# Kernel tuning notes

Measured on AMD Instinct MI355X. Metric: run time of the kernel, lower is better.

The kernel has to match this reference:

```python
import jax, jax.numpy as jnp
import numpy as np

SIZE_IN = 4096
SIZE_OUT = 4096
COEF = 8


def _make_mask(size_in, size_out, coef):
    # block-diagonal canceler: output row block i sees input column block i
    inp_sec = size_in // coef
    out_sec = size_out // coef
    row_block = np.arange(size_out) // out_sec  # [size_out]
    col_block = np.arange(size_in) // inp_sec   # [size_in]
    return (row_block[:, None] == col_block[None, :]).astype(np.float32)


def setup_inputs() -> dict:
    key = jax.random.key(0)
    kx, kw, kb = jax.random.split(key, 3)
    x = jax.random.normal(kx, (16384, SIZE_IN), dtype=jnp.float32)
    # kaiming_uniform_(a=sqrt(5)) on [size_out, size_in]: bound = sqrt(6/((1+5)*fan_in)) = 1/sqrt(fan_in)
    bound_w = 1.0 / np.sqrt(SIZE_IN)
    weights = jax.random.uniform(kw, (SIZE_OUT, SIZE_IN), minval=-bound_w, maxval=bound_w, dtype=jnp.float32)
    bound_b = 1.0 / np.sqrt(SIZE_IN)
    bias = jax.random.uniform(kb, (SIZE_OUT,), minval=-bound_b, maxval=bound_b, dtype=jnp.float32)
    mask = jnp.asarray(_make_mask(SIZE_IN, SIZE_OUT, COEF))
    return {"x": x, "weights": weights, "bias": bias, "mask": mask}


def reference(x, weights, bias, mask):
    # faithful to torch: full dense GEMM on the masked weight
    w = weights * mask                      # [size_out, size_in]
    return x @ w.T + bias                   # [batch, size_out]
```

## Files before the change

### kernel.cpp

```cpp
#include <hip/hip_runtime.h>
#include <hip/hip_bf16.h>


typedef __bf16 bf16x8 __attribute__((ext_vector_type(8)));
typedef float  f32x4  __attribute__((ext_vector_type(4)));

constexpr int LD = 4096;

__device__ __forceinline__ bf16x8 cvt8(f32x4 u, f32x4 v) {
    bf16x8 p;
    p[0] = (__bf16)u[0]; p[1] = (__bf16)u[1]; p[2] = (__bf16)u[2]; p[3] = (__bf16)u[3];
    p[4] = (__bf16)v[0]; p[5] = (__bf16)v[1]; p[6] = (__bf16)v[2]; p[7] = (__bf16)v[3];
    return p;
}

__device__ __forceinline__ void gload64(f32x4& a, f32x4& b, f32x4& c, f32x4& d,
                                        const void* p) {
    asm volatile("global_load_dwordx4 %0, %4, off\n\t"
                 "global_load_dwordx4 %1, %4, off offset:16\n\t"
                 "global_load_dwordx4 %2, %4, off offset:32\n\t"
                 "global_load_dwordx4 %3, %4, off offset:48"
                 : "=&v"(a), "=&v"(b), "=&v"(c), "=&v"(d) : "v"(p));
}
__device__ __forceinline__ void gload32(f32x4& a, f32x4& b, const void* p) {
    asm volatile("global_load_dwordx4 %0, %2, off\n\t"
                 "global_load_dwordx4 %1, %2, off offset:16"
                 : "=&v"(a), "=&v"(b) : "v"(p));
}

__global__ __launch_bounds__(256)
void pack_w(const float* __restrict__ w, __bf16* __restrict__ wt)
{
    const int g = blockIdx.x * 256 + threadIdx.x;
    const int base = g * 16;
    const int o = base >> 9;
    const int k = base & 511;
    const float* src = w + (size_t)o * LD + ((o >> 9) << 9) + k;
    f32x4 a = *(const f32x4*)(src);
    f32x4 b = *(const f32x4*)(src + 4);
    f32x4 c = *(const f32x4*)(src + 8);
    f32x4 d = *(const f32x4*)(src + 12);
    *(bf16x8*)(wt + base)     = cvt8(a, b);
    *(bf16x8*)(wt + base + 8) = cvt8(c, d);
}

#define VMW(N)                                                    \
    do {                                                          \
        asm volatile("s_waitcnt vmcnt(" #N ")" ::: "memory");     \
        __builtin_amdgcn_sched_barrier(0);                        \
    } while (0)

#define RD(TH, MH, KK)                                                        \
    do {                                                                      \
        const char* aB_ = smem + (TH) * 32768;                                \
        const char* bB_ = smem + 65536 + (TH) * 32768;                        \
        _Pragma("unroll")                                                     \
        for (int f = 0; f < 4; ++f) {                                         \
            const int row = wm * 128 + (MH) * 64 + f * 16 + arow;             \
            av[f] = *(const bf16x8*)(aB_ + row * 128 +                        \
                        (((KK) * 64 + ag * 16) ^ ((row & 7) << 4)));          \
        }                                                                     \
        _Pragma("unroll")                                                     \
        for (int n = 0; n < 4; ++n) {                                         \
            const int row = wn * 64 + n * 16 + arow;                          \
            bv[n] = *(const bf16x8*)(bB_ + row * 128 +                        \
                        (((KK) * 64 + ag * 16) ^ ((row & 7) << 4)));          \
        }                                                                     \
    } while (0)

#define FIRE(MH)                                                              \
    do {                                                                      \
        __builtin_amdgcn_s_barrier();                                         \
        asm volatile("s_waitcnt lgkmcnt(0)" ::: "memory");                    \
        __builtin_amdgcn_s_setprio(1);                                        \
        _Pragma("unroll")                                                     \
        for (int f = 0; f < 4; ++f)                                           \
            _Pragma("unroll")                                                 \
            for (int n = 0; n < 4; ++n)                                       \
                acc[(MH) * 4 + f][n] = __builtin_amdgcn_mfma_f32_16x16x32_bf16( \
                    av[f], bv[n], acc[(MH) * 4 + f][n], 0, 0, 0);             \
        __builtin_amdgcn_s_setprio(0);                                        \
        __builtin_amdgcn_s_barrier();                                         \
    } while (0)

__global__ __launch_bounds__(512, 2)
void fc_gemm(const float* __restrict__ x, const __bf16* __restrict__ wt,
             const float* __restrict__ bias, float* __restrict__ out)
{
    __shared__ __align__(16) char smem[131072];

    const int tid  = threadIdx.x;
    const int lane = tid & 63;
    const int wid  = tid >> 6;
    const int wm   = wid >> 2;
    const int wn   = wid & 3;

    const int bid  = blockIdx.x;
    const int j    = bid & 7;
    const int slot = bid >> 3;
    const int gm   = slot >> 1;
    const int gh   = slot & 1;
    const int koff    = j << 9;
    const int colbase = (j << 9) + (gh << 8);

    const int sRow = tid >> 2;
    const int sQ   = tid & 3;
    const int swzS = (sRow & 7) << 4;
    const int soA0 = sRow * 128 + ((sQ * 32)      ^ swzS);
    const int soA1 = sRow * 128 + ((sQ * 32 + 16) ^ swzS);
    const float*  xsB = x  + ((size_t)gm * 256 + sRow) * LD + koff + sQ * 16;
    const __bf16* wtB = wt + ((size_t)colbase + sRow) * 512 + sQ * 16;

    f32x4 stA[2][4];
    f32x4 stB[2][2];

    f32x4 acc[8][4];
#pragma unroll
    for (int i = 0; i < 8; ++i)
#pragma unroll
        for (int n = 0; n < 4; ++n)
            acc[i][n] = {0.f, 0.f, 0.f, 0.f};

    auto issueA = [&](int kt, int h) {
        gload64(stA[h][0], stA[h][1], stA[h][2], stA[h][3],
                xsB + (size_t)h * 128 * LD + kt * 64);
    };
    auto issueB = [&](int kt, int h) {
        gload32(stB[h][0], stB[h][1], wtB + (size_t)h * 65536 + kt * 64);
    };
    auto writeA = [&](int kt, int h) {
        char* base = smem + (kt & 1) * 32768 + h * 16384;
        *(bf16x8*)(base + soA0) = cvt8(stA[h][0], stA[h][1]);
        *(bf16x8*)(base + soA1) = cvt8(stA[h][2], stA[h][3]);
    };
    auto writeB = [&](int kt, int h) {
        char* base = smem + 65536 + (kt & 1) * 32768 + h * 16384;
        *(f32x4*)(base + soA0) = stB[h][0];
        *(f32x4*)(base + soA1) = stB[h][1];
    };

    const int arow = lane & 15;
    const int ag   = lane >> 4;
    bf16x8 av[4], bv[4];

    issueA(0, 0); issueA(0, 1); issueB(0, 0); issueB(0, 1);
    VMW(8); writeA(0, 0);
    VMW(4); writeA(0, 1);
    VMW(2); writeB(0, 0);
    VMW(0); writeB(0, 1);
    issueA(1, 0); issueA(1, 1);
    asm volatile("s_waitcnt lgkmcnt(0)" ::: "memory");
    __builtin_amdgcn_s_barrier();

    for (int i = 0; i < 3; ++i) {
        const int t1 = 2 * i + 1, t2 = 2 * i + 2, t3 = 2 * i + 3;
        { issueB(t1, 0); RD(0, 0, 0); VMW(6); writeA(t1, 0); FIRE(0); }
        { issueB(t1, 1); RD(0, 1, 0); VMW(4); writeA(t1, 1); FIRE(1); }
        { issueA(t2, 0); RD(0, 0, 1); VMW(6); writeB(t1, 0); FIRE(0); }
        { issueA(t2, 1); RD(0, 1, 1); VMW(8); writeB(t1, 1); FIRE(1); }
        { issueB(t2, 0); RD(1, 0, 0); VMW(6); writeA(t2, 0); FIRE(0); }
        { issueB(t2, 1); RD(1, 1, 0); VMW(4); writeA(t2, 1); FIRE(1); }
        { issueA(t3, 0); RD(1, 0, 1); VMW(6); writeB(t2, 0); FIRE(0); }
        { issueA(t3, 1); RD(1, 1, 1); VMW(8); writeB(t2, 1); FIRE(1); }
    }
    { issueB(7, 0); RD(0, 0, 0); VMW(6); writeA(7, 0); FIRE(0); }
    { issueB(7, 1); RD(0, 1, 0); VMW(4); writeA(7, 1); FIRE(1); }
    {               RD(0, 0, 1); VMW(2); writeB(7, 0); FIRE(0); }
    {               RD(0, 1, 1); VMW(0); writeB(7, 1); FIRE(1); }
    {               RD(1, 0, 0);                        FIRE(0); }
    {               RD(1, 1, 0);                        FIRE(1); }
    {               RD(1, 0, 1);                        FIRE(0); }
    {               RD(1, 1, 1);                        FIRE(1); }

    __syncthreads();

    float* pw = (float*)smem + wid * 1280;
    const int colg = colbase + wn * 64;
    const size_t rowg0 = (size_t)gm * 256 + wm * 128;
    float bv4[4];
#pragma unroll
    for (int n = 0; n < 4; ++n)
        bv4[n] = bias[colg + n * 16 + arow];

#pragma unroll
    for (int mi = 0; mi < 8; ++mi) {
#pragma unroll
        for (int n = 0; n < 4; ++n)
#pragma unroll
            for (int r2 = 0; r2 < 4; ++r2) {
                const int lr  = ag * 4 + r2;
                const int col = (n * 16 + arow) ^ ((lr & 12) << 2);
                pw[lr * 80 + col] = acc[mi][n][r2] + bv4[n];
            }
#pragma unroll
        for (int p = 0; p < 4; ++p) {
            const int q  = p * 64 + lane;
            const int lr = q >> 4;
            const int ci = q & 15;
            const f32x4 v4 = *(const f32x4*)(pw + lr * 80 + 4 * (ci ^ (lr & 12)));
            __builtin_nontemporal_store(v4,
                (f32x4*)(out + (rowg0 + mi * 16 + lr) * LD + colg + ci * 4));
        }
    }
}

extern "C" void kernel_launch(void* const* d_in, const int* in_sizes, int n_in,
                              void* d_out, int out_size, void* d_ws, size_t ws_size,
                              hipStream_t stream)
{
    const float* x    = (const float*)d_in[0];
    const float* wgt  = (const float*)d_in[1];
    const float* bias = (const float*)d_in[2];
    float* out = (float*)d_out;
    __bf16* wt = (__bf16*)d_ws;

    pack_w<<<dim3(512), dim3(256), 0, stream>>>(wgt, wt);
    fc_gemm<<<dim3(1024), dim3(512), 0, stream>>>(x, wt, bias, out);
}
```

Baseline: 131.8 us.

## Pre-swizzle packed weight tiles and stream them directly into LDS

```diff
diff --git a/kernel.cpp b/kernel.cpp
--- a/kernel.cpp
+++ b/kernel.cpp
@@ -22,26 +22,35 @@
                  "global_load_dwordx4 %3, %4, off offset:48"
                  : "=&v"(a), "=&v"(b), "=&v"(c), "=&v"(d) : "v"(p));
 }
-__device__ __forceinline__ void gload32(f32x4& a, f32x4& b, const void* p) {
-    asm volatile("global_load_dwordx4 %0, %2, off\n\t"
-                 "global_load_dwordx4 %1, %2, off offset:16"
-                 : "=&v"(a), "=&v"(b) : "v"(p));
+
+__device__ __forceinline__ void gload_lds16(const void* g, void* l) {
+    __builtin_amdgcn_global_load_lds(
+        (const __attribute__((address_space(1))) void*)g,
+        (__attribute__((address_space(3))) void*)l, 16, 0, 0);
 }
 
 __global__ __launch_bounds__(256)
-void pack_w(const float* __restrict__ w, __bf16* __restrict__ wt)
+void pack_w(const float* __restrict__ w, char* __restrict__ wtP)
 {
-    const int g = blockIdx.x * 256 + threadIdx.x;
-    const int base = g * 16;
-    const int o = base >> 9;
-    const int k = base & 511;
-    const float* src = w + (size_t)o * LD + ((o >> 9) << 9) + k;
+    const int g   = blockIdx.x * 256 + threadIdx.x;
+    const int col = g >> 5;
+    const int k16 = g & 31;
+    const int j   = col >> 9;
+    const int gh  = (col >> 8) & 1;
+    const int r   = col & 255;
+    const int kt  = k16 >> 2;
+    const int kq  = k16 & 3;
+    const int key = (r & 7) << 4;
+
+    const float* src = w + (size_t)col * LD + (j << 9) + kt * 64 + kq * 16;
     f32x4 a = *(const f32x4*)(src);
     f32x4 b = *(const f32x4*)(src + 4);
     f32x4 c = *(const f32x4*)(src + 8);
     f32x4 d = *(const f32x4*)(src + 12);
-    *(bf16x8*)(wt + base)     = cvt8(a, b);
-    *(bf16x8*)(wt + base + 8) = cvt8(c, d);
+
+    char* img = wtP + ((size_t)((j * 2 + gh) * 8 + kt)) * 32768 + r * 128;
+    *(bf16x8*)(img + ((kq * 32)      ^ key)) = cvt8(a, b);
+    *(bf16x8*)(img + ((kq * 32 + 16) ^ key)) = cvt8(c, d);
 }
 
 #define VMW(N)                                                    \
@@ -83,8 +92,24 @@
         __builtin_amdgcn_s_barrier();                                         \
     } while (0)
 
+#define FIRE_W(MH, N)                                                         \
+    do {                                                                      \
+        __builtin_amdgcn_s_barrier();                                         \
+        asm volatile("s_waitcnt lgkmcnt(0)" ::: "memory");                    \
+        __builtin_amdgcn_s_setprio(1);                                        \
+        _Pragma("unroll")                                                     \
+        for (int f = 0; f < 4; ++f)                                           \
+            _Pragma("unroll")                                                 \
+            for (int n = 0; n < 4; ++n)                                       \
+                acc[(MH) * 4 + f][n] = __builtin_amdgcn_mfma_f32_16x16x32_bf16( \
+                    av[f], bv[n], acc[(MH) * 4 + f][n], 0, 0, 0);             \
+        __builtin_amdgcn_s_setprio(0);                                        \
+        VMW(N);                                                               \
+        __builtin_amdgcn_s_barrier();                                         \
+    } while (0)
+
 __global__ __launch_bounds__(512, 2)
-void fc_gemm(const float* __restrict__ x, const __bf16* __restrict__ wt,
+void fc_gemm(const float* __restrict__ x, const char* __restrict__ wtP,
              const float* __restrict__ bias, float* __restrict__ out)
 {
     __shared__ __align__(16) char smem[131072];
@@ -102,17 +127,16 @@
     const int gh   = slot & 1;
     const int koff    = j << 9;
     const int colbase = (j << 9) + (gh << 8);
+    const int imgGrp  = (j * 2 + gh) * 8;
 
     const int sRow = tid >> 2;
     const int sQ   = tid & 3;
     const int swzS = (sRow & 7) << 4;
     const int soA0 = sRow * 128 + ((sQ * 32)      ^ swzS);
     const int soA1 = sRow * 128 + ((sQ * 32 + 16) ^ swzS);
-    const float*  xsB = x  + ((size_t)gm * 256 + sRow) * LD + koff + sQ * 16;
-    const __bf16* wtB = wt + ((size_t)colbase + sRow) * 512 + sQ * 16;
+    const float* xsB = x + ((size_t)gm * 256 + sRow) * LD + koff + sQ * 16;
 
     f32x4 stA[2][4];
-    f32x4 stB[2][2];
 
     f32x4 acc[8][4];
 #pragma unroll
@@ -124,53 +148,47 @@
     auto issueA = [&](int kt, int h) {
         gload64(stA[h][0], stA[h][1], stA[h][2], stA[h][3],
                 xsB + (size_t)h * 128 * LD + kt * 64);
-    };
-    auto issueB = [&](int kt, int h) {
-        gload32(stB[h][0], stB[h][1], wtB + (size_t)h * 65536 + kt * 64);
     };
     auto writeA = [&](int kt, int h) {
         char* base = smem + (kt & 1) * 32768 + h * 16384;
         *(bf16x8*)(base + soA0) = cvt8(stA[h][0], stA[h][1]);
         *(bf16x8*)(base + soA1) = cvt8(stA[h][2], stA[h][3]);
     };
-    auto writeB = [&](int kt, int h) {
-        char* base = smem + 65536 + (kt & 1) * 32768 + h * 16384;
-        *(f32x4*)(base + soA0) = stB[h][0];
-        *(f32x4*)(base + soA1) = stB[h][1];
+    auto issueB = [&](int kt) {
+        const char* src = wtP + (size_t)(imgGrp + kt) * 32768
+                        + wid * 4096 + lane * 16;
+        char* dst = smem + 65536 + (kt & 1) * 32768 + wid * 4096;
+#pragma unroll
+        for (int c = 0; c < 4; ++c)
+            gload_lds16(src + c * 1024, dst + c * 1024);
     };
 
     const int arow = lane & 15;
     const int ag   = lane >> 4;
     bf16x8 av[4], bv[4];
 
-    issueA(0, 0); issueA(0, 1); issueB(0, 0); issueB(0, 1);
-    VMW(8); writeA(0, 0);
-    VMW(4); writeA(0, 1);
-    VMW(2); writeB(0, 0);
-    VMW(0); writeB(0, 1);
-    issueA(1, 0); issueA(1, 1);
+    issueA(0, 0); issueA(0, 1); issueB(0);
+    VMW(8); writeA(0, 0); issueA(1, 0);
+    VMW(8); writeA(0, 1); issueA(1, 1);
+    VMW(8);
     asm volatile("s_waitcnt lgkmcnt(0)" ::: "memory");
     __builtin_amdgcn_s_barrier();
 
-    for (int i = 0; i < 3; ++i) {
-        const int t1 = 2 * i + 1, t2 = 2 * i + 2, t3 = 2 * i + 3;
-        { issueB(t1, 0); RD(0, 0, 0); VMW(6); writeA(t1, 0); FIRE(0); }
-        { issueB(t1, 1); RD(0, 1, 0); VMW(4); writeA(t1, 1); FIRE(1); }
-        { issueA(t2, 0); RD(0, 0, 1); VMW(6); writeB(t1, 0); FIRE(0); }
-        { issueA(t2, 1); RD(0, 1, 1); VMW(8); writeB(t1, 1); FIRE(1); }
-        { issueB(t2, 0); RD(1, 0, 0); VMW(6); writeA(t2, 0); FIRE(0); }
-        { issueB(t2, 1); RD(1, 1, 0); VMW(4); writeA(t2, 1); FIRE(1); }
-        { issueA(t3, 0); RD(1, 0, 1); VMW(6); writeB(t2, 0); FIRE(0); }
-        { issueA(t3, 1); RD(1, 1, 1); VMW(8); writeB(t2, 1); FIRE(1); }
+    for (int t = 0; t < 6; ++t) {
+        const int p = t & 1;
+        { issueB(t + 1); RD(p, 0, 0); FIRE(0); }
+        {                RD(p, 1, 0); FIRE(1); }
+        { RD(p, 0, 1); VMW(8); writeA(t + 1, 0); issueA(t + 2, 0); FIRE(0); }
+        { RD(p, 1, 1); VMW(8); writeA(t + 1, 1); issueA(t + 2, 1); FIRE_W(1, 8); }
     }
-    { issueB(7, 0); RD(0, 0, 0); VMW(6); writeA(7, 0); FIRE(0); }
-    { issueB(7, 1); RD(0, 1, 0); VMW(4); writeA(7, 1); FIRE(1); }
-    {               RD(0, 0, 1); VMW(2); writeB(7, 0); FIRE(0); }
-    {               RD(0, 1, 1); VMW(0); writeB(7, 1); FIRE(1); }
-    {               RD(1, 0, 0);                        FIRE(0); }
-    {               RD(1, 1, 0);                        FIRE(1); }
-    {               RD(1, 0, 1);                        FIRE(0); }
-    {               RD(1, 1, 1);                        FIRE(1); }
+    { issueB(7); RD(0, 0, 0); FIRE(0); }
+    {            RD(0, 1, 0); FIRE(1); }
+    { RD(0, 0, 1); VMW(8); writeA(7, 0); FIRE(0); }
+    { RD(0, 1, 1); VMW(4); writeA(7, 1); FIRE_W(1, 0); }
+    { RD(1, 0, 0); FIRE(0); }
+    { RD(1, 1, 0); FIRE(1); }
+    { RD(1, 0, 1); FIRE(0); }
+    { RD(1, 1, 1); FIRE(1); }
 
     __syncthreads();
 
@@ -212,8 +230,8 @@
     const float* wgt  = (const float*)d_in[1];
     const float* bias = (const float*)d_in[2];
     float* out = (float*)d_out;
-    __bf16* wt = (__bf16*)d_ws;
-
-    pack_w<<<dim3(512), dim3(256), 0, stream>>>(wgt, wt);
-    fc_gemm<<<dim3(1024), dim3(512), 0, stream>>>(x, wt, bias, out);
-}
+    char* wtP  = (char*)d_ws;
+
+    pack_w<<<dim3(512), dim3(256), 0, stream>>>(wgt, wtP);
+    fc_gemm<<<dim3(1024), dim3(512), 0, stream>>>(x, wtP, bias, out);
+}
```

Result: no change. 132.4 us (+0.4%).
